# Kernel tuning notes

Hardware: AMD Instinct MI355X
Metric: run time of the kernel (lower is better)

The kernel has to match this reference:

```python
import jax, jax.numpy as jnp
import numpy as np

B, S, D, H = 2, 4096, 256, 4
DH = D // H  # 64


def setup_inputs() -> dict:
    key = jax.random.key(0)
    ks = jax.random.split(key, 7)
    scale = 1.0 / np.sqrt(DH)  # torch Linear default init range ~ U(-1/sqrt(in), 1/sqrt(in))
    def w(k):
        return jax.random.uniform(k, (H, DH, DH), jnp.float32, -scale, scale)
    def b(k):
        return jax.random.uniform(k, (H, DH), jnp.float32, -scale, scale)
    return {
        "sequences": jax.random.normal(ks[0], (B, S, D), jnp.float32),
        "qw": w(ks[1]), "qb": b(ks[2]),
        "kw": w(ks[3]), "kb": b(ks[4]),
        "vw": w(ks[5]), "vb": b(ks[6]),
        "train": 0,
    }


def reference(sequences, qw, qb, kw, kb, vw, vb, train):
    # sequences: [B, S, D] -> per-head slices [B, H, S, DH]
    x = sequences.reshape(B, S, H, DH).transpose(0, 2, 1, 3)  # [B,H,S,DH]
    # torch Linear: y = x @ W.T + b, W: [out, in]
    q = jnp.einsum('bhsd,hed->bhse', x, qw) + qb[None, :, None, :]
    k = jnp.einsum('bhsd,hed->bhse', x, kw) + kb[None, :, None, :]
    v = jnp.einsum('bhsd,hed->bhse', x, vw) + vb[None, :, None, :]
    scores = jnp.einsum('bhqd,bhkd->bhqk', q, k) / jnp.sqrt(jnp.float32(DH))
    attn = jax.nn.softmax(scores, axis=-1)  # [B,H,S,S]
    out = jnp.einsum('bhqk,bhkd->bhqd', attn, v)  # [B,H,S,DH]
    # hstack over heads == concatenate head outputs along feature dim
    return out.transpose(0, 2, 1, 3).reshape(B, S, D)
```

## Files before the change

### kernel.cpp

```cpp
#include <hip/hip_runtime.h>
#include <hip/hip_bf16.h>


#define B_   2
#define S_   4096
#define D_   256
#define H_   4
#define DH_  64
#define BH_  8
#define NTOK (BH_*S_*DH_)

#define KVB  64
#define QW   32
#define NW   8
#define QB   (QW*NW)
#define NINST (BH_*(S_/QW))

typedef short v8s __attribute__((ext_vector_type(8)));
typedef float v16f __attribute__((ext_vector_type(16)));
typedef float v4f __attribute__((ext_vector_type(4)));
typedef unsigned v4u __attribute__((ext_vector_type(4)));
typedef unsigned v2u __attribute__((ext_vector_type(2)));
typedef int v2i __attribute__((ext_vector_type(2)));

#define QSCL (0.125f * 1.4426950408889634f)
#define DEFER_THR 8.0f

static __device__ __forceinline__ short f2bf(float f) {
    __hip_bfloat16 h = __float2bfloat16(f);
    return *reinterpret_cast<short*>(&h);
}
static __device__ __forceinline__ unsigned cvtpk(float lo, float hi) {
    unsigned r;
    asm("v_cvt_pk_bf16_f32 %0, %1, %2" : "=v"(r) : "v"(lo), "v"(hi));
    return r;
}
static __device__ __forceinline__ float fexp2(float x) {
#if __has_builtin(__builtin_amdgcn_exp2f)
    return __builtin_amdgcn_exp2f(x);
#else
    float r;
    asm("v_exp_f32 %0, %1" : "=v"(r) : "v"(x));
    return r;
#endif
}
static __device__ __forceinline__ float max3f(float a, float b, float c) {
    return fmaxf(fmaxf(a, b), c);
}
static __device__ __forceinline__ void pl32swap(unsigned &a, unsigned &b) {
#if __has_builtin(__builtin_amdgcn_permlane32_swap)
    v2i r = __builtin_amdgcn_permlane32_swap((int)a, (int)b, false, false);
    a = (unsigned)r[0]; b = (unsigned)r[1];
#else
    asm volatile("v_permlane32_swap_b32 %0, %1" : "+v"(a), "+v"(b));
#endif
}
static __device__ __forceinline__ float xmax32(float x) {
    unsigned a = __builtin_bit_cast(unsigned, x), b = a;
    pl32swap(a, b);
    return fmaxf(__builtin_bit_cast(float, a), __builtin_bit_cast(float, b));
}
static __device__ __forceinline__ float xadd32(float x) {
    unsigned a = __builtin_bit_cast(unsigned, x), b = a;
    pl32swap(a, b);
    return __builtin_bit_cast(float, a) + __builtin_bit_cast(float, b);
}
static __device__ __forceinline__ v16f vz16() {
    v16f z;
    #pragma unroll
    for (int i = 0; i < 16; ++i) z[i] = 0.f;
    return z;
}
static __device__ __forceinline__ v8s cvt8(const float* p) {
    v4f f0 = *(const v4f*)(p);
    v4f f1 = *(const v4f*)(p + 4);
    v4u u = { cvtpk(f0[0], f0[1]), cvtpk(f0[2], f0[3]),
              cvtpk(f1[0], f1[1]), cvtpk(f1[2], f1[3]) };
    return __builtin_bit_cast(v8s, u);
}

__global__ __launch_bounds__(128) void qkv_proj_mfma(
    const float* __restrict__ x,
    const float* __restrict__ qw, const float* __restrict__ qb,
    const float* __restrict__ kw, const float* __restrict__ kb,
    const float* __restrict__ vw, const float* __restrict__ vb,
    short* __restrict__ Qo, short* __restrict__ Ko, short* __restrict__ Vt)
{
    const int t   = threadIdx.x;
    const int w   = t >> 6;
    const int l   = t & 63;
    const int l31 = l & 31, lhi = l >> 5;
    const int bh  = blockIdx.y, h = bh & 3, b = bh >> 2;
    const int s0  = blockIdx.x * 32;

    const float* xrow = x + ((size_t)(b*S_ + s0 + l31))*D_ + h*DH_;
    v8s af[4];
    #pragma unroll
    for (int k0 = 0; k0 < 4; ++k0)
        af[k0] = cvt8(xrow + k0*16 + lhi*8);

    const float* Wp[3] = { qw + h*DH_*DH_, kw + h*DH_*DH_, vw + h*DH_*DH_ };
    const float* Bp[3] = { qb + h*DH_,     kb + h*DH_,     vb + h*DH_ };
    short* Qh = Qo + (size_t)bh*S_*DH_;
    short* Kh = Ko + (size_t)bh*S_*DH_;

    #pragma unroll
    for (int ui = 0; ui < 3; ++ui) {
        const int u  = w*3 + ui;
        const int p  = u >> 1;
        const int eb = u & 1;
        const int e  = eb*32 + l31;
        const float* wrow = Wp[p] + e*DH_;

        v16f acc = vz16();
        #pragma unroll
        for (int k0 = 0; k0 < 4; ++k0) {
            v8s bfr = cvt8(wrow + k0*16 + lhi*8);
            acc = __builtin_amdgcn_mfma_f32_32x32x16_bf16(af[k0], bfr, acc, 0, 0, 0);
        }

        const float bias = Bp[p][e];
        if (p == 0) {
            const float bq = bias * QSCL;
            #pragma unroll
            for (int r = 0; r < 16; ++r) acc[r] = fmaf(acc[r], QSCL, bq);
        } else {
            #pragma unroll
            for (int r = 0; r < 16; ++r) acc[r] += bias;
        }

        if (p < 2) {
            short* dst = (p == 0) ? Qh : Kh;
            #pragma unroll
            for (int r = 0; r < 16; ++r) {
                int s = s0 + (r & 3) + 8*(r >> 2) + 4*lhi;
                dst[(size_t)s*DH_ + e] = f2bf(acc[r]);
            }
        } else {
            short* vtb = Vt + (size_t)bh*DH_*S_ + (size_t)e*S_;
            #pragma unroll
            for (int rq = 0; rq < 4; ++rq) {
                v2u pr = { cvtpk(acc[rq*4+0], acc[rq*4+1]),
                           cvtpk(acc[rq*4+2], acc[rq*4+3]) };
                int s = s0 + rq*8 + 4*lhi;
                *(v2u*)(vtb + s) = pr;
            }
        }
    }
}

__global__ __launch_bounds__(512, 4) void attn_kernel(
    const short* __restrict__ Q, const short* __restrict__ K,
    const short* __restrict__ Vt, float* __restrict__ Opart,
    float* __restrict__ Ml, int nspl, int kvlen)
{
    __shared__ __align__(16) short klds[4][64][64];
    __shared__ __align__(16) short vlds[4][64][64];

    const int t    = threadIdx.x;
    const int w    = t >> 6;
    const int l    = t & 63;
    const int l31  = l & 31;
    const int lhi  = l >> 5;
    const int bh   = blockIdx.y;
    const int qtil = blockIdx.x;
    const int spl  = blockIdx.z;
    const int q0   = qtil*QB + w*QW;
    const int kv_beg = spl * kvlen;

    const short* Qh = Q  + (size_t)bh*S_*DH_;
    const short* Kh = K  + (size_t)bh*S_*DH_;
    const short* Vh = Vt + (size_t)bh*DH_*S_;

    const int rl  = l >> 3;
    const int cs  = (l & 7) ^ (rl & 7);
    const size_t koff = (size_t)(w*8 + rl)*DH_ + cs*8;
    const size_t voff = (size_t)(w*8 + rl)*S_  + cs*8;
    const int ldst = w*512 + l*8;

    v8s qf[4];
    #pragma unroll
    for (int k0 = 0; k0 < 4; ++k0)
        qf[k0] = *(const v8s*)(Qh + (size_t)(q0 + l31)*DH_ + k0*16 + lhi*8);

    int fo[2][4];
    #pragma unroll
    for (int a = 0; a < 2; ++a)
        #pragma unroll
        for (int c = 0; c < 4; ++c)
            fo[a][c] = (a*32 + l31)*64 + (((c*2 + lhi) ^ (l31 & 7))*8);

    v16f o0 = vz16(), o1 = vz16();
    float m_run = -INFINITY, l_run = 0.f;

    const int NT = kvlen / KVB;

    auto stage_direct = [&](int tile, int buf) {
        const size_t kvo = kv_beg + (size_t)tile*KVB;
        v8s kv = *(const v8s*)(Kh + kvo*DH_ + koff);
        v8s vv = *(const v8s*)(Vh + kvo      + voff);
        *(v8s*)((short*)klds + buf*4096 + ldst) = kv;
        *(v8s*)((short*)vlds + buf*4096 + ldst) = vv;
    };

    auto tilebody = [&](int buf) {
        const short* kb = (const short*)klds + buf*4096;
        const short* vb = (const short*)vlds + buf*4096;

        v16f s0 = vz16(), s1 = vz16();
        __builtin_amdgcn_s_setprio(1);
        #pragma unroll
        for (int k0 = 0; k0 < 4; ++k0) {
            v8s a0 = *(const v8s*)(kb + fo[0][k0]);
            v8s a1 = *(const v8s*)(kb + fo[1][k0]);
            s0 = __builtin_amdgcn_mfma_f32_32x32x16_bf16(a0, qf[k0], s0, 0, 0, 0);
            s1 = __builtin_amdgcn_mfma_f32_32x32x16_bf16(a1, qf[k0], s1, 0, 0, 0);
        }
        __builtin_amdgcn_s_setprio(0);

        float t16[16];
        #pragma unroll
        for (int i = 0; i < 16; ++i) t16[i] = fmaxf(s0[i], s1[i]);
        float r0 = max3f(t16[0],  t16[1],  t16[2]);
        float r1 = max3f(t16[3],  t16[4],  t16[5]);
        float r2 = max3f(t16[6],  t16[7],  t16[8]);
        float r3 = max3f(t16[9],  t16[10], t16[11]);
        float r4 = max3f(t16[12], t16[13], t16[14]);
        float mx = fmaxf(max3f(max3f(r0, r1, r2), r3, r4), t16[15]);
        mx = xmax32(mx);

        if (__any(mx > m_run + DEFER_THR)) {
            float mn = fmaxf(m_run, mx);
            float sc = fexp2(m_run - mn);
            #pragma unroll
            for (int i = 0; i < 16; ++i) { o0[i] *= sc; o1[i] *= sc; }
            l_run *= sc;
            m_run = mn;
        }
        #pragma unroll
        for (int i = 0; i < 16; ++i) s0[i] = fexp2(s0[i] - m_run);
        #pragma unroll
        for (int i = 0; i < 16; ++i) s1[i] = fexp2(s1[i] - m_run);
        float a16[16];
        #pragma unroll
        for (int i = 0; i < 16; ++i) a16[i] = s0[i] + s1[i];
        #pragma unroll
        for (int st = 8; st; st >>= 1)
            #pragma unroll
            for (int i = 0; i < st; ++i) a16[i] += a16[i+st];
        l_run += xadd32(a16[0]);

        unsigned pwv[4][4];
        {
            unsigned j0 = cvtpk(s0[0], s0[1]),  j1 = cvtpk(s0[2], s0[3]);
            unsigned j2 = cvtpk(s0[4], s0[5]),  j3 = cvtpk(s0[6], s0[7]);
            unsigned j4 = cvtpk(s0[8], s0[9]),  j5 = cvtpk(s0[10], s0[11]);
            unsigned j6 = cvtpk(s0[12], s0[13]), j7 = cvtpk(s0[14], s0[15]);
            pl32swap(j0, j2); pl32swap(j1, j3);
            pwv[0][0] = j0; pwv[0][1] = j1; pwv[0][2] = j2; pwv[0][3] = j3;
            pl32swap(j4, j6); pl32swap(j5, j7);
            pwv[1][0] = j4; pwv[1][1] = j5; pwv[1][2] = j6; pwv[1][3] = j7;
        }
        {
            unsigned j0 = cvtpk(s1[0], s1[1]),  j1 = cvtpk(s1[2], s1[3]);
            unsigned j2 = cvtpk(s1[4], s1[5]),  j3 = cvtpk(s1[6], s1[7]);
            unsigned j4 = cvtpk(s1[8], s1[9]),  j5 = cvtpk(s1[10], s1[11]);
            unsigned j6 = cvtpk(s1[12], s1[13]), j7 = cvtpk(s1[14], s1[15]);
            pl32swap(j0, j2); pl32swap(j1, j3);
            pwv[2][0] = j0; pwv[2][1] = j1; pwv[2][2] = j2; pwv[2][3] = j3;
            pl32swap(j4, j6); pl32swap(j5, j7);
            pwv[3][0] = j4; pwv[3][1] = j5; pwv[3][2] = j6; pwv[3][3] = j7;
        }

        __builtin_amdgcn_s_setprio(1);
        #pragma unroll
        for (int kk = 0; kk < 4; ++kk) {
            v4u u = { pwv[kk][0], pwv[kk][1], pwv[kk][2], pwv[kk][3] };
            v8s pf = __builtin_bit_cast(v8s, u);
            v8s va0 = *(const v8s*)(vb + fo[0][kk]);
            v8s va1 = *(const v8s*)(vb + fo[1][kk]);
            o0 = __builtin_amdgcn_mfma_f32_32x32x16_bf16(va0, pf, o0, 0, 0, 0);
            o1 = __builtin_amdgcn_mfma_f32_32x32x16_bf16(va1, pf, o1, 0, 0, 0);
        }
        __builtin_amdgcn_s_setprio(0);
    };

    stage_direct(0, 0);
    stage_direct(1, 1);
    __syncthreads();

    for (int it = 0; it < NT; it += 2) {
        v8s k2, v2;
        if (it + 2 < NT) {
            size_t kvn = kv_beg + (size_t)(it+2)*KVB;
            k2 = *(const v8s*)(Kh + kvn*DH_ + koff);
            v2 = *(const v8s*)(Vh + kvn + voff);
        }
        tilebody(it & 3);
        if (it + 2 < NT) {
            *(v8s*)((short*)klds + ((it+2)&3)*4096 + ldst) = k2;
            *(v8s*)((short*)vlds + ((it+2)&3)*4096 + ldst) = v2;
        }
        v8s k3, v3;
        if (it + 3 < NT) {
            size_t kvn = kv_beg + (size_t)(it+3)*KVB;
            k3 = *(const v8s*)(Kh + kvn*DH_ + koff);
            v3 = *(const v8s*)(Vh + kvn + voff);
        }
        tilebody((it + 1) & 3);
        if (it + 3 < NT) {
            *(v8s*)((short*)klds + ((it+3)&3)*4096 + ldst) = k3;
            *(v8s*)((short*)vlds + ((it+3)&3)*4096 + ldst) = v3;
        }
        __syncthreads();
    }

    const int inst = bh*(S_/QW) + qtil*NW + w;
    float* od = Opart + ((size_t)inst*nspl + spl)*2048;
    #pragma unroll
    for (int r = 0; r < 16; ++r) od[r*64 + l]      = o0[r];
    #pragma unroll
    for (int r = 0; r < 16; ++r) od[(16+r)*64 + l] = o1[r];
    Ml[((size_t)inst*nspl + spl)*64 + l] = (l < 32) ? m_run : l_run;
}

template<int NSPL>
__global__ __launch_bounds__(256) void combine_kernel(
    const float* __restrict__ Opart, const float* __restrict__ Ml,
    float* __restrict__ out)
{
    const int t = threadIdx.x;
    const int w = t >> 6, l = t & 63;
    const int inst = blockIdx.x*4 + w;
    const int bh = inst >> 7;
    const int qw = inst & 127;
    const int b = bh >> 2, h = bh & 3;
    const int l31 = l & 31, lhi = l >> 5;
    const int q = qw*32 + l31;

    const float* mlp = Ml + (size_t)inst*NSPL*64;
    float m[NSPL], lv[NSPL];
    float M = -INFINITY;
    #pragma unroll
    for (int sp = 0; sp < NSPL; ++sp) {
        m[sp]  = mlp[sp*64 + l31];
        lv[sp] = mlp[sp*64 + 32 + l31];
        M = fmaxf(M, m[sp]);
    }
    float wgt[NSPL], L = 0.f;
    #pragma unroll
    for (int sp = 0; sp < NSPL; ++sp) {
        wgt[sp] = fexp2(m[sp] - M);
        L += lv[sp] * wgt[sp];
    }
    float inv = 1.f / L;

    const float* op0 = Opart + (size_t)inst*NSPL*2048;
    float* outp = out + ((size_t)(b*S_ + q))*D_ + h*DH_;

    #pragma unroll
    for (int g = 0; g < 8; ++g) {
        v4f acc;
        #pragma unroll
        for (int jj = 0; jj < 4; ++jj) {
            int r = g*4 + jj;
            float v = 0.f;
            #pragma unroll
            for (int sp = 0; sp < NSPL; ++sp)
                v += op0[sp*2048 + r*64 + l] * wgt[sp];
            acc[jj] = v * inv;
        }
        int td = g >> 2, gg = g & 3;
        int d = td*32 + gg*8 + lhi*4;
        *(v4f*)(outp + d) = acc;
    }
}

extern "C" void kernel_launch(void* const* d_in, const int* in_sizes, int n_in,
                              void* d_out, int out_size, void* d_ws, size_t ws_size,
                              hipStream_t stream)
{
    const float* x  = (const float*)d_in[0];
    const float* qw = (const float*)d_in[1];
    const float* qb = (const float*)d_in[2];
    const float* kw = (const float*)d_in[3];
    const float* kb = (const float*)d_in[4];
    const float* vw = (const float*)d_in[5];
    const float* vb = (const float*)d_in[6];

    short* Qb  = (short*)d_ws;
    short* Kb  = Qb + NTOK;
    short* Vtb = Kb + NTOK;
    float* Opart = (float*)(Vtb + NTOK);

    size_t base = (size_t)3*NTOK*sizeof(short);
    size_t per_spl = (size_t)NINST*2048*4 + (size_t)NINST*64*4;
    int nspl = 1;
    if      (ws_size >= base + 4*per_spl) nspl = 4;
    else if (ws_size >= base + 2*per_spl) nspl = 2;
    float* Ml = Opart + (size_t)NINST*nspl*2048;
    int kvlen = S_/nspl;

    float* out = (float*)d_out;

    dim3 pg(S_/32, BH_), pb(128);
    hipLaunchKernelGGL(qkv_proj_mfma, pg, pb, 0, stream,
                       x, qw, qb, kw, kb, vw, vb, Qb, Kb, Vtb);

    dim3 ag(S_/QB, BH_, nspl), ab(512);
    hipLaunchKernelGGL(attn_kernel, ag, ab, 0, stream, Qb, Kb, Vtb, Opart, Ml, nspl, kvlen);

    dim3 cg(NINST/4), cb(256);
    if (nspl == 4)
        hipLaunchKernelGGL(combine_kernel<4>, cg, cb, 0, stream, Opart, Ml, out);
    else if (nspl == 2)
        hipLaunchKernelGGL(combine_kernel<2>, cg, cb, 0, stream, Opart, Ml, out);
    else
        hipLaunchKernelGGL(combine_kernel<1>, cg, cb, 0, stream, Opart, Ml, out);
}
```

Baseline: 74.23 us.

## Ping-pong QK^T and softmax/PV phases between two wave groups

Splits the fused tile body into a QK^T phase and a softmax+PV phase. Waves are divided into two groups that run the phases out of step, with a barrier between phases, so matrix-core work in one group can overlap softmax ALU work in the other. The main loop now handles one KV tile per iteration with two barriers each, and the second group finishes with a trailing softmax+PV. This adds barriers, and the 4-buffer prefetch ring must stay consistent because the lagging group reads the previous tile's buffer.

```diff
diff --git a/kernel.cpp b/kernel.cpp
--- a/kernel.cpp
+++ b/kernel.cpp
@@ -191,23 +191,14 @@
             fo[a][c] = (a*32 + l31)*64 + (((c*2 + lhi) ^ (l31 & 7))*8);
 
     v16f o0 = vz16(), o1 = vz16();
+    v16f s0, s1;
     float m_run = -INFINITY, l_run = 0.f;
 
     const int NT = kvlen / KVB;
 
-    auto stage_direct = [&](int tile, int buf) {
-        const size_t kvo = kv_beg + (size_t)tile*KVB;
-        v8s kv = *(const v8s*)(Kh + kvo*DH_ + koff);
-        v8s vv = *(const v8s*)(Vh + kvo      + voff);
-        *(v8s*)((short*)klds + buf*4096 + ldst) = kv;
-        *(v8s*)((short*)vlds + buf*4096 + ldst) = vv;
-    };
-
-    auto tilebody = [&](int buf) {
+    auto qkt = [&](int buf) {
         const short* kb = (const short*)klds + buf*4096;
-        const short* vb = (const short*)vlds + buf*4096;
-
-        v16f s0 = vz16(), s1 = vz16();
+        s0 = vz16(); s1 = vz16();
         __builtin_amdgcn_s_setprio(1);
         #pragma unroll
         for (int k0 = 0; k0 < 4; ++k0) {
@@ -217,6 +208,10 @@
             s1 = __builtin_amdgcn_mfma_f32_32x32x16_bf16(a1, qf[k0], s1, 0, 0, 0);
         }
         __builtin_amdgcn_s_setprio(0);
+    };
+
+    auto smpv = [&](int buf) {
+        const short* vb = (const short*)vlds + buf*4096;
 
         float t16[16];
         #pragma unroll
@@ -285,35 +280,42 @@
         __builtin_amdgcn_s_setprio(0);
     };
 
-    stage_direct(0, 0);
-    stage_direct(1, 1);
+    {
+        v8s k0v = *(const v8s*)(Kh + (size_t)kv_beg*DH_ + koff);
+        v8s v0v = *(const v8s*)(Vh + kv_beg + voff);
+        *(v8s*)((short*)klds + ldst) = k0v;
+        *(v8s*)((short*)vlds + ldst) = v0v;
+        v8s k1v = *(const v8s*)(Kh + ((size_t)kv_beg + KVB)*DH_ + koff);
+        v8s v1v = *(const v8s*)(Vh + kv_beg + KVB + voff);
+        *(v8s*)((short*)klds + 4096 + ldst) = k1v;
+        *(v8s*)((short*)vlds + 4096 + ldst) = v1v;
+    }
     __syncthreads();
 
-    for (int it = 0; it < NT; it += 2) {
+    const bool gA = (w < 4);
+
+    for (int it = 0; it < NT; ++it) {
         v8s k2, v2;
-        if (it + 2 < NT) {
+        const bool pf = (it + 2 < NT);
+        if (pf) {
             size_t kvn = kv_beg + (size_t)(it+2)*KVB;
             k2 = *(const v8s*)(Kh + kvn*DH_ + koff);
             v2 = *(const v8s*)(Vh + kvn + voff);
         }
-        tilebody(it & 3);
-        if (it + 2 < NT) {
+
+        if (gA)          qkt(it & 3);
+        else if (it > 0) smpv((it-1) & 3);
+        __syncthreads();
+        if (gA) smpv(it & 3);
+        else    qkt(it & 3);
+
+        if (pf) {
             *(v8s*)((short*)klds + ((it+2)&3)*4096 + ldst) = k2;
             *(v8s*)((short*)vlds + ((it+2)&3)*4096 + ldst) = v2;
         }
-        v8s k3, v3;
-        if (it + 3 < NT) {
-            size_t kvn = kv_beg + (size_t)(it+3)*KVB;
-            k3 = *(const v8s*)(Kh + kvn*DH_ + koff);
-            v3 = *(const v8s*)(Vh + kvn + voff);
-        }
-        tilebody((it + 1) & 3);
-        if (it + 3 < NT) {
-            *(v8s*)((short*)klds + ((it+3)&3)*4096 + ldst) = k3;
-            *(v8s*)((short*)vlds + ((it+3)&3)*4096 + ldst) = v3;
-        }
         __syncthreads();
     }
+    if (!gA) smpv((NT-1) & 3);
 
     const int inst = bh*(S_/QW) + qtil*NW + w;
     float* od = Opart + ((size_t)inst*nspl + spl)*2048;
```

Result: slower. 80.78 us (+8.8%).
